# Optimization experiments

Measured on AMD Instinct MI355X. Metric: run time of the kernel, lower is better.

## Reference

```python
import jax, jax.numpy as jnp
import numpy as np

N = 50000
E = 1600000
IN, OUT = 128, 64


def _gcn(h, W, b, src, dst):
    # DGL GraphConv, norm='both', weight applied first (in>out), activation=relu
    x = h @ W  # [N, OUT]
    ones = jnp.ones((src.shape[0],), dtype=h.dtype)
    deg_out = jnp.clip(jax.ops.segment_sum(ones, src, num_segments=N), 1.0)
    deg_in = jnp.clip(jax.ops.segment_sum(ones, dst, num_segments=N), 1.0)
    x = x * jax.lax.rsqrt(deg_out)[:, None]
    agg = jax.ops.segment_sum(x[src], dst, num_segments=N)  # SpMM
    agg = agg * jax.lax.rsqrt(deg_in)[:, None]
    return jax.nn.relu(agg + b)


def setup_inputs() -> dict:
    key = jax.random.key(0)
    ks = jax.random.split(key, 10)
    inp = {"h": jax.random.normal(ks[0], (N, IN), dtype=jnp.float32)}
    for i in range(3):
        inp[f"src{i}"] = jax.random.randint(ks[1 + 2 * i], (E,), 0, N, dtype=jnp.int32)
        inp[f"dst{i}"] = jax.random.randint(ks[2 + 2 * i], (E,), 0, N, dtype=jnp.int32)
        inp[f"W{i}"] = jax.random.normal(ks[7 + i], (IN, OUT), dtype=jnp.float32) * (1.0 / np.sqrt(IN))
        inp[f"b{i}"] = jnp.zeros((OUT,), dtype=jnp.float32)
    return inp


def reference(h, src0, dst0, src1, dst1, src2, dst2, W0, b0, W1, b1, W2, b2):
    e0 = _gcn(h, W0, b0, src0, dst0)
    e1 = _gcn(h, W1, b1, src1, dst1)
    e2 = _gcn(h, W2, b2, src2, dst2)
    # stack over meta-path dim then mean == average of semantic embeddings
    return (e0 + e1 + e2) / 3.0
```

## Files before the change

### kernel.cpp

```cpp
#include <hip/hip_runtime.h>

#define KDIM 128
#define NCOLS 64
#define NCHUNK 64
#define NRANGE 2
#define RBINS 25088
#define RWORDS (RBINS / 2)
#define CWORDS (NRANGE * RWORDS)
#define BUCKET 64
#define NBUCK 782
#define CAP 2560
#define NPB 85

struct GArgs {
  const int*   src[3];
  const int*   dst[3];
  const float* W[3];
  const float* b[3];
  int          E[3];
};

__device__ __forceinline__ unsigned short f2bf(float f) {
  unsigned u = __float_as_uint(f);
  u += 0x7FFFu + ((u >> 16) & 1u);
  return (unsigned short)(u >> 16);
}
__device__ __forceinline__ float bflo(unsigned u) { return __uint_as_float(u << 16); }
__device__ __forceinline__ float bfhi(unsigned u) { return __uint_as_float(u & 0xFFFF0000u); }

__global__ __launch_bounds__(256) void partition_all_kernel(
    GArgs A, int* __restrict__ bucket_cur, unsigned* __restrict__ P2) {
  __shared__ int lcnt[NBUCK];
  __shared__ int lcur[NBUCK];
  const int g = blockIdx.y;
  const int E = A.E[g];
  const int per_block = (((E + NPB - 1) / NPB) + 3) & ~3;
  const int* __restrict__ src = A.src[g];
  const int* __restrict__ dst = A.dst[g];
  int* __restrict__ bcur = bucket_cur + g * NBUCK;
  unsigned* __restrict__ P2g = P2 + (size_t)g * NBUCK * CAP;

  const int t = threadIdx.x;
  const int e0 = blockIdx.x * per_block;
  const int e1 = min(e0 + per_block, E);
  const int n = max(e1 - e0, 0);
  const int nv = n >> 2;
  const int4* d4 = (const int4*)&dst[e0];
  const int4* s4 = (const int4*)&src[e0];
  for (int i = t; i < NBUCK; i += 256) lcnt[i] = 0;
  __syncthreads();
  for (int v = t; v < nv; v += 256) {
    int4 d = d4[v];
    atomicAdd(&lcnt[(unsigned)d.x >> 6], 1);
    atomicAdd(&lcnt[(unsigned)d.y >> 6], 1);
    atomicAdd(&lcnt[(unsigned)d.z >> 6], 1);
    atomicAdd(&lcnt[(unsigned)d.w >> 6], 1);
  }
  for (int e = e0 + (nv << 2) + t; e < e1; e += 256)
    atomicAdd(&lcnt[(unsigned)dst[e] >> 6], 1);
  __syncthreads();
  for (int i = t; i < NBUCK; i += 256) {
    int c = lcnt[i];
    lcur[i] = c ? atomicAdd(&bcur[i], c) : 0;
  }
  __syncthreads();
  for (int v = t; v < nv; v += 256) {
    int4 d = d4[v];
    int4 s = s4[v];
    unsigned bk; int pos;
    bk = (unsigned)d.x >> 6;
    pos = atomicAdd(&lcur[bk], 1);
    if (pos < CAP) P2g[(size_t)bk * CAP + pos] = (unsigned)s.x | (((unsigned)d.x & 63u) << 16);
    bk = (unsigned)d.y >> 6;
    pos = atomicAdd(&lcur[bk], 1);
    if (pos < CAP) P2g[(size_t)bk * CAP + pos] = (unsigned)s.y | (((unsigned)d.y & 63u) << 16);
    bk = (unsigned)d.z >> 6;
    pos = atomicAdd(&lcur[bk], 1);
    if (pos < CAP) P2g[(size_t)bk * CAP + pos] = (unsigned)s.z | (((unsigned)d.z & 63u) << 16);
    bk = (unsigned)d.w >> 6;
    pos = atomicAdd(&lcur[bk], 1);
    if (pos < CAP) P2g[(size_t)bk * CAP + pos] = (unsigned)s.w | (((unsigned)d.w & 63u) << 16);
  }
  for (int e = e0 + (nv << 2) + t; e < e1; e += 256) {
    unsigned d = (unsigned)dst[e];
    unsigned bk = d >> 6;
    int pos = atomicAdd(&lcur[bk], 1);
    if (pos < CAP) P2g[(size_t)bk * CAP + pos] = (unsigned)src[e] | ((d & 63u) << 16);
  }
}

__global__ __launch_bounds__(256) void hist_all_kernel(
    GArgs A, unsigned* __restrict__ P) {
  __shared__ unsigned hist[RWORDS];
  const int g = blockIdx.z;
  const int E = A.E[g];
  const int per_chunk = (((E + NCHUNK - 1) / NCHUNK) + 3) & ~3;
  const int* __restrict__ keys = A.src[g];
  unsigned* __restrict__ Pg = P + (size_t)g * NCHUNK * CWORDS;

  const int chunk = blockIdx.x;
  const int base  = blockIdx.y * RBINS;
  const int t = threadIdx.x;
  for (int i = t; i < RWORDS; i += 256) hist[i] = 0;
  __syncthreads();
  const int e0 = chunk * per_chunk;
  const int e1 = min(e0 + per_chunk, E);
  const int n = max(e1 - e0, 0);
  const int nv = n >> 2;
  const int4* k4p = (const int4*)&keys[e0];
  for (int v = t; v < nv; v += 256) {
    int4 k4 = k4p[v];
    unsigned k0 = (unsigned)(k4.x - base);
    unsigned k1 = (unsigned)(k4.y - base);
    unsigned k2 = (unsigned)(k4.z - base);
    unsigned k3 = (unsigned)(k4.w - base);
    if (k0 < (unsigned)RBINS) atomicAdd(&hist[k0 >> 1], 1u << ((k0 & 1u) * 16));
    if (k1 < (unsigned)RBINS) atomicAdd(&hist[k1 >> 1], 1u << ((k1 & 1u) * 16));
    if (k2 < (unsigned)RBINS) atomicAdd(&hist[k2 >> 1], 1u << ((k2 & 1u) * 16));
    if (k3 < (unsigned)RBINS) atomicAdd(&hist[k3 >> 1], 1u << ((k3 & 1u) * 16));
  }
  for (int e = e0 + (nv << 2) + t; e < e1; e += 256) {
    unsigned k = (unsigned)(keys[e] - base);
    if (k < (unsigned)RBINS) atomicAdd(&hist[k >> 1], 1u << ((k & 1u) * 16));
  }
  __syncthreads();
  unsigned* dstp = Pg + (size_t)chunk * CWORDS + blockIdx.y * RWORDS;
  for (int i = t; i < RWORDS; i += 256) dstp[i] = hist[i];
}

__device__ __forceinline__ void fma4(float4& a, float s, const float4& b) {
  a.x = fmaf(s, b.x, a.x);
  a.y = fmaf(s, b.y, a.y);
  a.z = fmaf(s, b.z, a.z);
  a.w = fmaf(s, b.w, a.w);
}

__global__ __launch_bounds__(256) void gemm_all_kernel(
    GArgs A, const float* __restrict__ h, const unsigned* __restrict__ P,
    unsigned short* __restrict__ x, int N) {
  __shared__ float Ws[KDIM * NCOLS];
  __shared__ int ldeg[128];

  const int g = blockIdx.y;
  const float* __restrict__ W = A.W[g];
  const unsigned* __restrict__ Pg = P + (size_t)g * NCHUNK * CWORDS;
  unsigned short* __restrict__ xg = x + (size_t)g * N * NCOLS;

  const int t = threadIdx.x;
  const int tx = t & 15;
  const int ty = t >> 4;
  const int row0 = blockIdx.x * 128;

  #pragma unroll
  for (int i = 0; i < 8; ++i) {
    int lin = i * 1024 + t * 4;
    *(float4*)&Ws[lin] = *(const float4*)&W[lin];
  }
  {
    int lrow = t >> 1;
    int part = t & 1;
    int row = min(row0 + lrow, N - 1);
    int word = row >> 1;
    int shift = (row & 1) * 16;
    int s = 0;
    #pragma unroll
    for (int c = 0; c < 32; ++c)
      s += (int)((Pg[(size_t)(part * 32 + c) * CWORDS + word] >> shift) & 0xFFFFu);
    ldeg[lrow] = 0;
    __syncthreads();
    atomicAdd(&ldeg[lrow], s);
  }
  __syncthreads();

  int r0 = row0 + 8 * ty;
  const float* hp[8];
  #pragma unroll
  for (int r = 0; r < 8; ++r) hp[r] = &h[(size_t)min(r0 + r, N - 1) * KDIM];

  float4 acc[8];
  #pragma unroll
  for (int r = 0; r < 8; ++r) acc[r] = make_float4(0.f, 0.f, 0.f, 0.f);

  #pragma unroll 2
  for (int k = 0; k < KDIM; k += 4) {
    float4 w0 = *(float4*)&Ws[(k + 0) * NCOLS + 4 * tx];
    float4 w1 = *(float4*)&Ws[(k + 1) * NCOLS + 4 * tx];
    float4 w2 = *(float4*)&Ws[(k + 2) * NCOLS + 4 * tx];
    float4 w3 = *(float4*)&Ws[(k + 3) * NCOLS + 4 * tx];
    #pragma unroll
    for (int r = 0; r < 8; ++r) {
      float4 a = *(const float4*)&hp[r][k];
      fma4(acc[r], a.x, w0);
      fma4(acc[r], a.y, w1);
      fma4(acc[r], a.z, w2);
      fma4(acc[r], a.w, w3);
    }
  }

  #pragma unroll
  for (int r = 0; r < 8; ++r) {
    int row = r0 + r;
    if (row < N) {
      float s = rsqrtf(fmaxf((float)ldeg[8 * ty + r], 1.0f));
      ushort4 o;
      o.x = f2bf(acc[r].x * s);
      o.y = f2bf(acc[r].y * s);
      o.z = f2bf(acc[r].z * s);
      o.w = f2bf(acc[r].w * s);
      *(ushort4*)&xg[(size_t)row * NCOLS + 4 * tx] = o;
    }
  }
}

__global__ __launch_bounds__(512) void spmm_all_kernel(
    GArgs A, const unsigned* __restrict__ P2, const int* __restrict__ bucket_cur,
    const unsigned short* __restrict__ x, float* __restrict__ out, int N) {
  __shared__ int cnt[BUCKET];
  __shared__ int rs[BUCKET + 1];
  __shared__ int cur[BUCKET];
  __shared__ int sd[BUCKET];
  __shared__ unsigned short srcs[CAP];

  const int t = threadIdx.x;
  const int bk = blockIdx.x;
  const int dbase = bk * BUCKET;
  const int nd = min(BUCKET, N - dbase);
  const int grp = t >> 3;
  const int qe = (t & 7) * 8;

  float tot[8];
  #pragma unroll
  for (int j = 0; j < 8; ++j) tot[j] = 0.f;

  for (int g = 0; g < 3; ++g) {
    const unsigned* __restrict__ P2b = P2 + ((size_t)g * NBUCK + bk) * CAP;
    const unsigned short* __restrict__ xg = x + (size_t)g * N * NCOLS;
    const int ne = min(bucket_cur[g * NBUCK + bk], CAP);

    __syncthreads();
    if (t < BUCKET) cnt[t] = 0;
    __syncthreads();
    for (int i = t; i < ne; i += 512)
      atomicAdd(&cnt[P2b[i] >> 16], 1);
    __syncthreads();
    int v = 0;
    if (t < BUCKET) { v = cnt[t]; sd[t] = v; }
    __syncthreads();
    #pragma unroll
    for (int off = 1; off < BUCKET; off <<= 1) {
      int add = (t < BUCKET && t >= off) ? sd[t - off] : 0;
      __syncthreads();
      if (t < BUCKET) sd[t] += add;
      __syncthreads();
    }
    if (t < BUCKET) { int ex = sd[t] - v; rs[t] = ex; cur[t] = ex; }
    if (t == 0) rs[BUCKET] = sd[BUCKET - 1];
    __syncthreads();
    for (int i = t; i < ne; i += 512) {
      unsigned p = P2b[i];
      int pos = atomicAdd(&cur[p >> 16], 1);
      srcs[pos] = (unsigned short)(p & 0xFFFFu);
    }
    __syncthreads();

    if (grp < nd) {
      int i = rs[grp];
      const int iend = rs[grp + 1];
      const int deg = iend - i;
      float acc[8];
      #pragma unroll
      for (int j = 0; j < 8; ++j) acc[j] = 0.f;
      for (; i + 3 < iend; i += 4) {
        int sa = srcs[i + 0];
        int sb = srcs[i + 1];
        int sc = srcs[i + 2];
        int sdd = srcs[i + 3];
        uint4 ua = *(const uint4*)&xg[(size_t)sa * NCOLS + qe];
        uint4 ub = *(const uint4*)&xg[(size_t)sb * NCOLS + qe];
        uint4 uc = *(const uint4*)&xg[(size_t)sc * NCOLS + qe];
        uint4 ud = *(const uint4*)&xg[(size_t)sdd * NCOLS + qe];
        acc[0] += bflo(ua.x) + bflo(ub.x) + bflo(uc.x) + bflo(ud.x);
        acc[1] += bfhi(ua.x) + bfhi(ub.x) + bfhi(uc.x) + bfhi(ud.x);
        acc[2] += bflo(ua.y) + bflo(ub.y) + bflo(uc.y) + bflo(ud.y);
        acc[3] += bfhi(ua.y) + bfhi(ub.y) + bfhi(uc.y) + bfhi(ud.y);
        acc[4] += bflo(ua.z) + bflo(ub.z) + bflo(uc.z) + bflo(ud.z);
        acc[5] += bfhi(ua.z) + bfhi(ub.z) + bfhi(uc.z) + bfhi(ud.z);
        acc[6] += bflo(ua.w) + bflo(ub.w) + bflo(uc.w) + bflo(ud.w);
        acc[7] += bfhi(ua.w) + bfhi(ub.w) + bfhi(uc.w) + bfhi(ud.w);
      }
      for (; i < iend; ++i) {
        int s = srcs[i];
        uint4 u = *(const uint4*)&xg[(size_t)s * NCOLS + qe];
        acc[0] += bflo(u.x); acc[1] += bfhi(u.x);
        acc[2] += bflo(u.y); acc[3] += bfhi(u.y);
        acc[4] += bflo(u.z); acc[5] += bfhi(u.z);
        acc[6] += bflo(u.w); acc[7] += bfhi(u.w);
      }
      float sc2 = rsqrtf(fmaxf((float)deg, 1.0f));
      const float* bg = A.b[g] + qe;
      #pragma unroll
      for (int j = 0; j < 8; ++j)
        tot[j] += fmaxf(fmaf(acc[j], sc2, bg[j]), 0.f) * (1.0f / 3.0f);
    }
  }

  if (grp < nd) {
    float* op = &out[(size_t)(dbase + grp) * NCOLS + qe];
    *(float4*)&op[0] = make_float4(tot[0], tot[1], tot[2], tot[3]);
    *(float4*)&op[4] = make_float4(tot[4], tot[5], tot[6], tot[7]);
  }
}

extern "C" void kernel_launch(void* const* d_in, const int* in_sizes, int n_in,
                              void* d_out, int out_size, void* d_ws, size_t ws_size,
                              hipStream_t stream) {
  const float* h = (const float*)d_in[0];
  const int N = in_sizes[0] / KDIM;
  float* out = (float*)d_out;

  GArgs A;
  for (int g = 0; g < 3; ++g) {
    A.src[g] = (const int*)  d_in[1 + g * 4];
    A.dst[g] = (const int*)  d_in[2 + g * 4];
    A.W[g]   = (const float*)d_in[3 + g * 4];
    A.b[g]   = (const float*)d_in[4 + g * 4];
    A.E[g]   = in_sizes[1 + g * 4];
  }

  char* w = (char*)d_ws;
  unsigned short* x = (unsigned short*)w;
  char*     w2 = w + (size_t)3 * N * NCOLS * sizeof(unsigned short);
  unsigned* P2 = (unsigned*)w2;
  char*     w3 = w2 + (size_t)3 * NBUCK * CAP * sizeof(unsigned);
  unsigned* P  = (unsigned*)w3;
  int* bucket_cur = (int*)(P + (size_t)3 * NCHUNK * CWORDS);

  hipMemsetAsync(bucket_cur, 0, 3 * NBUCK * sizeof(int), stream);
  partition_all_kernel<<<dim3(NPB, 3), 256, 0, stream>>>(A, bucket_cur, P2);
  hist_all_kernel<<<dim3(NCHUNK, NRANGE, 3), 256, 0, stream>>>(A, P);
  gemm_all_kernel<<<dim3((N + 127) / 128, 3), 256, 0, stream>>>(A, h, P, x, N);
  spmm_all_kernel<<<NBUCK, 512, 0, stream>>>(A, P2, bucket_cur, x, out, N);
}
```

Baseline: 311.3 us.

## Replace fixed-capacity bucket partition with two-level counting sort into CSR

Edges are now grouped by destination in two levels. A coarse count, scan and partition into 512-node ranges writes a compact edge array, then a fine in-block counting sort per range produces a CSR layout with row_start and a 16-bit source array. The SpMM kernel no longer runs its own per-bucket histogram, scan and scatter for each graph; it just loads row offsets and copies sorted sources into shared memory. This trades two extra small kernels and an extra pass over the edges for a simpler SpMM with fewer barriers and atomics.

```diff
diff --git a/kernel.cpp b/kernel.cpp
--- a/kernel.cpp
+++ b/kernel.cpp
@@ -7,9 +7,12 @@
 #define RBINS 25088
 #define RWORDS (RBINS / 2)
 #define CWORDS (NRANGE * RWORDS)
+#define COARSE 512
+#define NC 98
+#define SFCAP 17408
 #define BUCKET 64
 #define NBUCK 782
-#define CAP 2560
+#define FCAP 2816
 #define NPB 85
 
 struct GArgs {
@@ -28,65 +31,152 @@
 __device__ __forceinline__ float bflo(unsigned u) { return __uint_as_float(u << 16); }
 __device__ __forceinline__ float bfhi(unsigned u) { return __uint_as_float(u & 0xFFFF0000u); }
 
-__global__ __launch_bounds__(256) void partition_all_kernel(
-    GArgs A, int* __restrict__ bucket_cur, unsigned* __restrict__ P2) {
-  __shared__ int lcnt[NBUCK];
-  __shared__ int lcur[NBUCK];
+__global__ __launch_bounds__(256) void count_coarse_kernel(
+    GArgs A, int* __restrict__ tot) {
+  __shared__ int hcnt[NC];
+  const int g = blockIdx.y;
+  const int E = A.E[g];
+  const int per_block = (((E + NPB - 1) / NPB) + 3) & ~3;
+  const int* __restrict__ dst = A.dst[g];
+  const int t = threadIdx.x;
+  if (t < NC) hcnt[t] = 0;
+  __syncthreads();
+  const int e0 = blockIdx.x * per_block;
+  const int e1 = min(e0 + per_block, E);
+  const int n = max(e1 - e0, 0);
+  const int nv = n >> 2;
+  const int4* d4 = (const int4*)&dst[e0];
+  for (int v = t; v < nv; v += 256) {
+    int4 d = d4[v];
+    atomicAdd(&hcnt[(unsigned)d.x >> 9], 1);
+    atomicAdd(&hcnt[(unsigned)d.y >> 9], 1);
+    atomicAdd(&hcnt[(unsigned)d.z >> 9], 1);
+    atomicAdd(&hcnt[(unsigned)d.w >> 9], 1);
+  }
+  for (int e = e0 + (nv << 2) + t; e < e1; e += 256)
+    atomicAdd(&hcnt[(unsigned)dst[e] >> 9], 1);
+  __syncthreads();
+  if (t < NC && hcnt[t]) atomicAdd(&tot[g * NC + t], hcnt[t]);
+}
+
+__global__ __launch_bounds__(128) void scan_off_kernel(
+    const int* __restrict__ tot, int* __restrict__ off, int* __restrict__ cursor) {
+  __shared__ int sd[128];
+  const int t = threadIdx.x;
+  for (int g = 0; g < 3; ++g) {
+    int v = (t < NC) ? tot[g * NC + t] : 0;
+    sd[t] = v;
+    __syncthreads();
+    for (int o = 1; o < 128; o <<= 1) {
+      int add = (t >= o) ? sd[t - o] : 0;
+      __syncthreads();
+      sd[t] += add;
+      __syncthreads();
+    }
+    int excl = sd[t] - v;
+    if (t < NC) { off[g * (NC + 1) + t] = excl; cursor[g * NC + t] = excl; }
+    if (t == 0) off[g * (NC + 1) + NC] = sd[127];
+    __syncthreads();
+  }
+}
+
+__global__ __launch_bounds__(256) void partition_coarse_kernel(
+    GArgs A, int* __restrict__ cursor, unsigned* __restrict__ P2c, int Emax) {
+  __shared__ int lcnt[NC];
+  __shared__ int lcur[NC];
   const int g = blockIdx.y;
   const int E = A.E[g];
   const int per_block = (((E + NPB - 1) / NPB) + 3) & ~3;
   const int* __restrict__ src = A.src[g];
   const int* __restrict__ dst = A.dst[g];
-  int* __restrict__ bcur = bucket_cur + g * NBUCK;
-  unsigned* __restrict__ P2g = P2 + (size_t)g * NBUCK * CAP;
-
-  const int t = threadIdx.x;
+  unsigned* __restrict__ P2g = P2c + (size_t)g * Emax;
+  const int t = threadIdx.x;
+  if (t < NC) lcnt[t] = 0;
+  __syncthreads();
   const int e0 = blockIdx.x * per_block;
   const int e1 = min(e0 + per_block, E);
   const int n = max(e1 - e0, 0);
   const int nv = n >> 2;
   const int4* d4 = (const int4*)&dst[e0];
   const int4* s4 = (const int4*)&src[e0];
-  for (int i = t; i < NBUCK; i += 256) lcnt[i] = 0;
-  __syncthreads();
   for (int v = t; v < nv; v += 256) {
     int4 d = d4[v];
-    atomicAdd(&lcnt[(unsigned)d.x >> 6], 1);
-    atomicAdd(&lcnt[(unsigned)d.y >> 6], 1);
-    atomicAdd(&lcnt[(unsigned)d.z >> 6], 1);
-    atomicAdd(&lcnt[(unsigned)d.w >> 6], 1);
+    atomicAdd(&lcnt[(unsigned)d.x >> 9], 1);
+    atomicAdd(&lcnt[(unsigned)d.y >> 9], 1);
+    atomicAdd(&lcnt[(unsigned)d.z >> 9], 1);
+    atomicAdd(&lcnt[(unsigned)d.w >> 9], 1);
   }
   for (int e = e0 + (nv << 2) + t; e < e1; e += 256)
-    atomicAdd(&lcnt[(unsigned)dst[e] >> 6], 1);
-  __syncthreads();
-  for (int i = t; i < NBUCK; i += 256) {
-    int c = lcnt[i];
-    lcur[i] = c ? atomicAdd(&bcur[i], c) : 0;
+    atomicAdd(&lcnt[(unsigned)dst[e] >> 9], 1);
+  __syncthreads();
+  if (t < NC) {
+    int c = lcnt[t];
+    lcur[t] = c ? atomicAdd(&cursor[g * NC + t], c) : 0;
   }
   __syncthreads();
   for (int v = t; v < nv; v += 256) {
     int4 d = d4[v];
     int4 s = s4[v];
     unsigned bk; int pos;
-    bk = (unsigned)d.x >> 6;
-    pos = atomicAdd(&lcur[bk], 1);
-    if (pos < CAP) P2g[(size_t)bk * CAP + pos] = (unsigned)s.x | (((unsigned)d.x & 63u) << 16);
-    bk = (unsigned)d.y >> 6;
-    pos = atomicAdd(&lcur[bk], 1);
-    if (pos < CAP) P2g[(size_t)bk * CAP + pos] = (unsigned)s.y | (((unsigned)d.y & 63u) << 16);
-    bk = (unsigned)d.z >> 6;
-    pos = atomicAdd(&lcur[bk], 1);
-    if (pos < CAP) P2g[(size_t)bk * CAP + pos] = (unsigned)s.z | (((unsigned)d.z & 63u) << 16);
-    bk = (unsigned)d.w >> 6;
-    pos = atomicAdd(&lcur[bk], 1);
-    if (pos < CAP) P2g[(size_t)bk * CAP + pos] = (unsigned)s.w | (((unsigned)d.w & 63u) << 16);
+    bk = (unsigned)d.x >> 9; pos = atomicAdd(&lcur[bk], 1);
+    P2g[pos] = (unsigned)s.x | (((unsigned)d.x & 511u) << 16);
+    bk = (unsigned)d.y >> 9; pos = atomicAdd(&lcur[bk], 1);
+    P2g[pos] = (unsigned)s.y | (((unsigned)d.y & 511u) << 16);
+    bk = (unsigned)d.z >> 9; pos = atomicAdd(&lcur[bk], 1);
+    P2g[pos] = (unsigned)s.z | (((unsigned)d.z & 511u) << 16);
+    bk = (unsigned)d.w >> 9; pos = atomicAdd(&lcur[bk], 1);
+    P2g[pos] = (unsigned)s.w | (((unsigned)d.w & 511u) << 16);
   }
   for (int e = e0 + (nv << 2) + t; e < e1; e += 256) {
     unsigned d = (unsigned)dst[e];
-    unsigned bk = d >> 6;
+    unsigned bk = d >> 9;
     int pos = atomicAdd(&lcur[bk], 1);
-    if (pos < CAP) P2g[(size_t)bk * CAP + pos] = (unsigned)src[e] | ((d & 63u) << 16);
-  }
+    P2g[pos] = (unsigned)src[e] | ((d & 511u) << 16);
+  }
+}
+
+__global__ __launch_bounds__(512) void sort_fine_kernel(
+    const unsigned* __restrict__ P2c, const int* __restrict__ off,
+    unsigned short* __restrict__ S, int* __restrict__ row_start,
+    int N, int Emax) {
+  __shared__ int cnt[COARSE];
+  __shared__ int sd[COARSE];
+  __shared__ int cur[COARSE];
+  __shared__ unsigned short outl[SFCAP];
+  const int c = blockIdx.x;
+  const int g = blockIdx.y;
+  const unsigned* __restrict__ P2g = P2c + (size_t)g * Emax;
+  const int base_e = off[g * (NC + 1) + c];
+  const int nloc = off[g * (NC + 1) + c + 1] - base_e;
+  const int t = threadIdx.x;
+
+  cnt[t] = 0;
+  __syncthreads();
+  for (int i = t; i < nloc; i += 512)
+    atomicAdd(&cnt[(P2g[base_e + i] >> 16) & 511u], 1);
+  __syncthreads();
+  int v = cnt[t];
+  sd[t] = v;
+  __syncthreads();
+  for (int o = 1; o < 512; o <<= 1) {
+    int add = (t >= o) ? sd[t - o] : 0;
+    __syncthreads();
+    sd[t] += add;
+    __syncthreads();
+  }
+  int excl = sd[t] - v;
+  cur[t] = excl;
+  int node = c * COARSE + t;
+  if (node <= N) row_start[g * (N + 1) + node] = base_e + excl;
+  __syncthreads();
+  for (int i = t; i < nloc; i += 512) {
+    unsigned p = P2g[base_e + i];
+    int pos = atomicAdd(&cur[(p >> 16) & 511u], 1);
+    if (pos < SFCAP) outl[pos] = (unsigned short)(p & 0xFFFFu);
+  }
+  __syncthreads();
+  unsigned short* __restrict__ Sg = S + (size_t)g * Emax;
+  for (int i = t; i < nloc; i += 512) Sg[base_e + i] = outl[i];
 }
 
 __global__ __launch_bounds__(256) void hist_all_kernel(
@@ -213,13 +303,11 @@
 }
 
 __global__ __launch_bounds__(512) void spmm_all_kernel(
-    GArgs A, const unsigned* __restrict__ P2, const int* __restrict__ bucket_cur,
-    const unsigned short* __restrict__ x, float* __restrict__ out, int N) {
-  __shared__ int cnt[BUCKET];
+    GArgs A, const unsigned short* __restrict__ S,
+    const int* __restrict__ row_start, const unsigned short* __restrict__ x,
+    float* __restrict__ out, int N, int Emax) {
   __shared__ int rs[BUCKET + 1];
-  __shared__ int cur[BUCKET];
-  __shared__ int sd[BUCKET];
-  __shared__ unsigned short srcs[CAP];
+  __shared__ unsigned short srcs[FCAP];
 
   const int t = threadIdx.x;
   const int bk = blockIdx.x;
@@ -233,39 +321,21 @@
   for (int j = 0; j < 8; ++j) tot[j] = 0.f;
 
   for (int g = 0; g < 3; ++g) {
-    const unsigned* __restrict__ P2b = P2 + ((size_t)g * NBUCK + bk) * CAP;
+    const unsigned short* __restrict__ Sg = S + (size_t)g * Emax;
+    const int* __restrict__ rsg = row_start + (size_t)g * (N + 1);
     const unsigned short* __restrict__ xg = x + (size_t)g * N * NCOLS;
-    const int ne = min(bucket_cur[g * NBUCK + bk], CAP);
-
-    __syncthreads();
-    if (t < BUCKET) cnt[t] = 0;
-    __syncthreads();
-    for (int i = t; i < ne; i += 512)
-      atomicAdd(&cnt[P2b[i] >> 16], 1);
-    __syncthreads();
-    int v = 0;
-    if (t < BUCKET) { v = cnt[t]; sd[t] = v; }
-    __syncthreads();
-    #pragma unroll
-    for (int off = 1; off < BUCKET; off <<= 1) {
-      int add = (t < BUCKET && t >= off) ? sd[t - off] : 0;
-      __syncthreads();
-      if (t < BUCKET) sd[t] += add;
-      __syncthreads();
-    }
-    if (t < BUCKET) { int ex = sd[t] - v; rs[t] = ex; cur[t] = ex; }
-    if (t == 0) rs[BUCKET] = sd[BUCKET - 1];
-    __syncthreads();
-    for (int i = t; i < ne; i += 512) {
-      unsigned p = P2b[i];
-      int pos = atomicAdd(&cur[p >> 16], 1);
-      srcs[pos] = (unsigned short)(p & 0xFFFFu);
-    }
+
+    __syncthreads();
+    if (t <= BUCKET) rs[t] = rsg[min(dbase + t, N)];
+    __syncthreads();
+    const int e0 = rs[0];
+    const int ne = min(rs[BUCKET] - e0, FCAP);
+    for (int i = t; i < ne; i += 512) srcs[i] = Sg[e0 + i];
     __syncthreads();
 
     if (grp < nd) {
-      int i = rs[grp];
-      const int iend = rs[grp + 1];
+      int i = rs[grp] - e0;
+      const int iend = min(rs[grp + 1] - e0, ne);
       const int deg = iend - i;
       float acc[8];
       #pragma unroll
@@ -319,25 +389,36 @@
   float* out = (float*)d_out;
 
   GArgs A;
+  int Emax = 0;
   for (int g = 0; g < 3; ++g) {
     A.src[g] = (const int*)  d_in[1 + g * 4];
     A.dst[g] = (const int*)  d_in[2 + g * 4];
     A.W[g]   = (const float*)d_in[3 + g * 4];
     A.b[g]   = (const float*)d_in[4 + g * 4];
     A.E[g]   = in_sizes[1 + g * 4];
+    if (A.E[g] > Emax) Emax = A.E[g];
   }
 
   char* w = (char*)d_ws;
   unsigned short* x = (unsigned short*)w;
   char*     w2 = w + (size_t)3 * N * NCOLS * sizeof(unsigned short);
-  unsigned* P2 = (unsigned*)w2;
-  char*     w3 = w2 + (size_t)3 * NBUCK * CAP * sizeof(unsigned);
+  unsigned* P2c = (unsigned*)w2;
+  char*     w3 = w2 + (size_t)3 * Emax * sizeof(unsigned);
   unsigned* P  = (unsigned*)w3;
-  int* bucket_cur = (int*)(P + (size_t)3 * NCHUNK * CWORDS);
-
-  hipMemsetAsync(bucket_cur, 0, 3 * NBUCK * sizeof(int), stream);
-  partition_all_kernel<<<dim3(NPB, 3), 256, 0, stream>>>(A, bucket_cur, P2);
+  char*     w4 = w3 + (size_t)3 * NCHUNK * CWORDS * sizeof(unsigned);
+  int* row_start = (int*)w4;
+  char*     w5 = w4 + (size_t)3 * (N + 1) * sizeof(int);
+  int* tot    = (int*)w5;
+  int* off    = tot + 3 * NC;
+  int* cursor = off + 3 * (NC + 1);
+  unsigned short* S = (unsigned short*)(cursor + 3 * NC + 2);
+
+  hipMemsetAsync(tot, 0, 3 * NC * sizeof(int), stream);
+  count_coarse_kernel<<<dim3(NPB, 3), 256, 0, stream>>>(A, tot);
+  scan_off_kernel<<<1, 128, 0, stream>>>(tot, off, cursor);
+  partition_coarse_kernel<<<dim3(NPB, 3), 256, 0, stream>>>(A, cursor, P2c, Emax);
+  sort_fine_kernel<<<dim3(NC, 3), 512, 0, stream>>>(P2c, off, S, row_start, N, Emax);
   hist_all_kernel<<<dim3(NCHUNK, NRANGE, 3), 256, 0, stream>>>(A, P);
   gemm_all_kernel<<<dim3((N + 127) / 128, 3), 256, 0, stream>>>(A, h, P, x, N);
-  spmm_all_kernel<<<NBUCK, 512, 0, stream>>>(A, P2, bucket_cur, x, out, N);
-}
+  spmm_all_kernel<<<NBUCK, 512, 0, stream>>>(A, S, row_start, x, out, N, Emax);
+}
```

Result: slower. 319.8 us (+2.7%).
